# Performance work log

Measured on AMD Instinct MI355X. Metric: run time of the kernel, lower is better.

The kernel has to match this reference:

```python
import jax, jax.numpy as jnp
import numpy as np

COMMITMENT_COST = 0.25


def setup_inputs() -> dict:
    key = jax.random.key(0)
    k1, k2 = jax.random.split(key)
    B, K, D = 1048576, 16, 64
    z = jax.random.normal(k1, (B, D), dtype=jnp.float32)
    # nn.Embedding init: uniform(-1/K, 1/K)
    embedding = jax.random.uniform(k2, (K, D), dtype=jnp.float32,
                                   minval=-1.0 / K, maxval=1.0 / K)
    return {"z": z, "embedding": embedding}


def reference(z, embedding):
    # squared L2 distances: ||z||^2 + ||e||^2 - 2 z e^T  -> [B, K]
    distances = (jnp.sum(z * z, axis=1, keepdims=True)
                 + jnp.sum(embedding * embedding, axis=1)
                 - 2.0 * jnp.matmul(z, embedding.T))
    encoding_indices = jnp.argmin(distances, axis=1)           # [B]
    quantized = embedding[encoding_indices]                    # [B, D]

    commitment_loss = jnp.mean((z - jax.lax.stop_gradient(quantized)) ** 2)
    embedding_loss = jnp.mean((jax.lax.stop_gradient(z) - quantized) ** 2)
    vq_loss = embedding_loss + COMMITMENT_COST * commitment_loss

    # straight-through estimator
    quantized = z + jax.lax.stop_gradient(quantized - z)
    return quantized, encoding_indices, vq_loss
```

## Files before the change

### kernel.cpp

```cpp
#include <hip/hip_runtime.h>

#define B_ROWS 1048576
#define K_CODES 16
#define D_DIM 64

constexpr int BLOCK = 256;
constexpr int GRID  = 2048;

__global__ __launch_bounds__(BLOCK)
void vq_main(const float* __restrict__ z,
             const float* __restrict__ emb,
             float* __restrict__ out_q,
             float* __restrict__ out_idx,
             float* __restrict__ partials)
{
    __shared__ __align__(16) float s_emb[K_CODES * D_DIM];
    __shared__ float s_se[K_CODES];
    __shared__ float s_w[BLOCK / 64];

    const int t = threadIdx.x;

    ((float4*)s_emb)[t] = ((const float4*)emb)[t];
    __syncthreads();

    if (t < K_CODES) {
        float s = 0.f;
        #pragma unroll
        for (int c = 0; c < D_DIM; ++c) {
            float e = s_emb[t * D_DIM + c];
            s = fmaf(e, e, s);
        }
        s_se[t] = s;
    }
    __syncthreads();

    const int j = t & 15;
    float4 ereg[16];
    #pragma unroll
    for (int k = 0; k < 16; ++k)
        ereg[k] = *(const float4*)&s_emb[k * D_DIM + j * 4];
    const float se_j = s_se[j];

    float lossacc = 0.f;

    const int gid    = (blockIdx.x * BLOCK + t) >> 4;
    const int stride = (GRID * BLOCK) >> 4;

    for (int row = gid; row < B_ROWS; row += stride) {
        const float4 zv = *(const float4*)&z[(size_t)row * D_DIM + j * 4];

        float p[16];
        #pragma unroll
        for (int k = 0; k < 16; ++k) {
            float4 e = ereg[k];
            p[k] = fmaf(zv.w, e.w, fmaf(zv.z, e.z, fmaf(zv.y, e.y, zv.x * e.x)));
        }
        float szp = fmaf(zv.w, zv.w, fmaf(zv.z, zv.z, fmaf(zv.y, zv.y, zv.x * zv.x)));
        szp += __shfl_xor(szp, 8, 64);
        szp += __shfl_xor(szp, 4, 64);
        szp += __shfl_xor(szp, 2, 64);
        szp += __shfl_xor(szp, 1, 64);

        bool hi = (j & 8) != 0;
        float r8[8];
        #pragma unroll
        for (int i = 0; i < 8; ++i) {
            float sendv = hi ? p[i] : p[i + 8];
            float keepv = hi ? p[i + 8] : p[i];
            r8[i] = keepv + __shfl_xor(sendv, 8, 64);
        }
        hi = (j & 4) != 0;
        float r4[4];
        #pragma unroll
        for (int i = 0; i < 4; ++i) {
            float sendv = hi ? r8[i] : r8[i + 4];
            float keepv = hi ? r8[i + 4] : r8[i];
            r4[i] = keepv + __shfl_xor(sendv, 4, 64);
        }
        hi = (j & 2) != 0;
        float r2[2];
        #pragma unroll
        for (int i = 0; i < 2; ++i) {
            float sendv = hi ? r2[i] : r4[i + 2];
            (void)sendv;
        }
        {
            float sendv0 = hi ? r4[0] : r4[2];
            float keepv0 = hi ? r4[2] : r4[0];
            r2[0] = keepv0 + __shfl_xor(sendv0, 2, 64);
            float sendv1 = hi ? r4[1] : r4[3];
            float keepv1 = hi ? r4[3] : r4[1];
            r2[1] = keepv1 + __shfl_xor(sendv1, 2, 64);
        }
        hi = (j & 1) != 0;
        float dot;
        {
            float sendv = hi ? r2[0] : r2[1];
            float keepv = hi ? r2[1] : r2[0];
            dot = keepv + __shfl_xor(sendv, 1, 64);
        }

        const float tt = szp + se_j;
        const float d  = tt - 2.0f * dot;

        float vmin = d;
        vmin = fminf(vmin, __shfl_xor(vmin, 1, 64));
        vmin = fminf(vmin, __shfl_xor(vmin, 2, 64));
        vmin = fminf(vmin, __shfl_xor(vmin, 4, 64));
        vmin = fminf(vmin, __shfl_xor(vmin, 8, 64));
        unsigned long long bal = __ballot(d == vmin);
        unsigned int mask = (unsigned int)((bal >> (t & 48)) & 0xFFFFull);
        int kmin = __ffs(mask) - 1;

        const float4 qv = *(const float4*)&s_emb[kmin * D_DIM + j * 4];

        float dx = zv.x - qv.x; lossacc = fmaf(dx, dx, lossacc);
        dx = zv.y - qv.y;       lossacc = fmaf(dx, dx, lossacc);
        dx = zv.z - qv.z;       lossacc = fmaf(dx, dx, lossacc);
        dx = zv.w - qv.w;       lossacc = fmaf(dx, dx, lossacc);

        *(float4*)&out_q[(size_t)row * D_DIM + j * 4] = qv;
        if (j == 0) out_idx[row] = (float)kmin;
    }

    lossacc += __shfl_xor(lossacc, 32, 64);
    lossacc += __shfl_xor(lossacc, 16, 64);
    lossacc += __shfl_xor(lossacc, 8, 64);
    lossacc += __shfl_xor(lossacc, 4, 64);
    lossacc += __shfl_xor(lossacc, 2, 64);
    lossacc += __shfl_xor(lossacc, 1, 64);
    if ((t & 63) == 0) s_w[t >> 6] = lossacc;
    __syncthreads();
    if (t == 0) partials[blockIdx.x] = (s_w[0] + s_w[1]) + (s_w[2] + s_w[3]);
}

__global__ void vq_finalize(const float* __restrict__ partials, int n,
                            float* __restrict__ out_loss)
{
    __shared__ float sw[4];
    float s = 0.f;
    for (int i = threadIdx.x; i < n; i += 256) s += partials[i];
    s += __shfl_xor(s, 32, 64);
    s += __shfl_xor(s, 16, 64);
    s += __shfl_xor(s, 8, 64);
    s += __shfl_xor(s, 4, 64);
    s += __shfl_xor(s, 2, 64);
    s += __shfl_xor(s, 1, 64);
    if ((threadIdx.x & 63) == 0) sw[threadIdx.x >> 6] = s;
    __syncthreads();
    if (threadIdx.x == 0) {
        float tot = (sw[0] + sw[1]) + (sw[2] + sw[3]);
        *out_loss = tot * (1.25f / (float)(B_ROWS * (size_t)D_DIM));
    }
}

extern "C" void kernel_launch(void* const* d_in, const int* in_sizes, int n_in,
                              void* d_out, int out_size, void* d_ws, size_t ws_size,
                              hipStream_t stream)
{
    const float* z   = (const float*)d_in[0];
    const float* emb = (const float*)d_in[1];
    float* out      = (float*)d_out;
    float* out_q    = out;
    float* out_idx  = out + (size_t)B_ROWS * D_DIM;
    float* out_loss = out_idx + B_ROWS;
    float* partials = (float*)d_ws;

    vq_main<<<GRID, BLOCK, 0, stream>>>(z, emb, out_q, out_idx, partials);
    vq_finalize<<<1, 256, 0, stream>>>(partials, GRID, out_loss);
}
```

Before: 122.8 us.

## Use DPP/swizzle butterfly reduction with XOR-permuted codebook and prefetch next row

Cross-lane shuffles (ds_bpermute) are replaced with DPP quad-permutes for xor 1/2 and ds_swizzle for xor 4/8. The codebook registers are stored XOR-permuted by lane, so the transpose-reduction becomes a plain butterfly without select operations. The next row's z vector is software-prefetched into registers so its load overlaps the current row's compute. The kernel is memory-bound, so the lighter instruction work and the latency hiding may only help modestly. The extra prefetch registers add pressure on an already large register set.

Result: faster. 114.2 us (-7.1%).

```diff
diff --git a/kernel.cpp b/kernel.cpp
--- a/kernel.cpp
+++ b/kernel.cpp
@@ -6,6 +6,25 @@
 
 constexpr int BLOCK = 256;
 constexpr int GRID  = 2048;
+
+__device__ __forceinline__ float xor1_dpp(float x) {
+    return __builtin_bit_cast(float,
+        __builtin_amdgcn_update_dpp(0, __builtin_bit_cast(int, x), 0xB1 ,
+                                    0xF, 0xF, true));
+}
+__device__ __forceinline__ float xor2_dpp(float x) {
+    return __builtin_bit_cast(float,
+        __builtin_amdgcn_update_dpp(0, __builtin_bit_cast(int, x), 0x4E ,
+                                    0xF, 0xF, true));
+}
+__device__ __forceinline__ float xor4_sw(float x) {
+    return __builtin_bit_cast(float,
+        __builtin_amdgcn_ds_swizzle(__builtin_bit_cast(int, x), 0x101F));
+}
+__device__ __forceinline__ float xor8_sw(float x) {
+    return __builtin_bit_cast(float,
+        __builtin_amdgcn_ds_swizzle(__builtin_bit_cast(int, x), 0x201F));
+}
 
 __global__ __launch_bounds__(BLOCK)
 void vq_main(const float* __restrict__ z,
@@ -37,8 +56,8 @@
     const int j = t & 15;
     float4 ereg[16];
     #pragma unroll
-    for (int k = 0; k < 16; ++k)
-        ereg[k] = *(const float4*)&s_emb[k * D_DIM + j * 4];
+    for (int r = 0; r < 16; ++r)
+        ereg[r] = *(const float4*)&s_emb[((r ^ j) * D_DIM) + j * 4];
     const float se_j = s_se[j];
 
     float lossacc = 0.f;
@@ -46,68 +65,44 @@
     const int gid    = (blockIdx.x * BLOCK + t) >> 4;
     const int stride = (GRID * BLOCK) >> 4;
 
-    for (int row = gid; row < B_ROWS; row += stride) {
-        const float4 zv = *(const float4*)&z[(size_t)row * D_DIM + j * 4];
+    int row = gid;
+    float4 zv = *(const float4*)&z[(size_t)row * D_DIM + j * 4];
+
+    while (row < B_ROWS) {
+        const int nrow = row + stride;
+        float4 zn = zv;
+        if (nrow < B_ROWS)
+            zn = *(const float4*)&z[(size_t)nrow * D_DIM + j * 4];
 
         float p[16];
         #pragma unroll
-        for (int k = 0; k < 16; ++k) {
-            float4 e = ereg[k];
-            p[k] = fmaf(zv.w, e.w, fmaf(zv.z, e.z, fmaf(zv.y, e.y, zv.x * e.x)));
-        }
-        float szp = fmaf(zv.w, zv.w, fmaf(zv.z, zv.z, fmaf(zv.y, zv.y, zv.x * zv.x)));
-        szp += __shfl_xor(szp, 8, 64);
-        szp += __shfl_xor(szp, 4, 64);
-        szp += __shfl_xor(szp, 2, 64);
-        szp += __shfl_xor(szp, 1, 64);
-
-        bool hi = (j & 8) != 0;
-        float r8[8];
-        #pragma unroll
-        for (int i = 0; i < 8; ++i) {
-            float sendv = hi ? p[i] : p[i + 8];
-            float keepv = hi ? p[i + 8] : p[i];
-            r8[i] = keepv + __shfl_xor(sendv, 8, 64);
-        }
-        hi = (j & 4) != 0;
-        float r4[4];
-        #pragma unroll
-        for (int i = 0; i < 4; ++i) {
-            float sendv = hi ? r8[i] : r8[i + 4];
-            float keepv = hi ? r8[i + 4] : r8[i];
-            r4[i] = keepv + __shfl_xor(sendv, 4, 64);
-        }
-        hi = (j & 2) != 0;
-        float r2[2];
-        #pragma unroll
-        for (int i = 0; i < 2; ++i) {
-            float sendv = hi ? r2[i] : r4[i + 2];
-            (void)sendv;
-        }
-        {
-            float sendv0 = hi ? r4[0] : r4[2];
-            float keepv0 = hi ? r4[2] : r4[0];
-            r2[0] = keepv0 + __shfl_xor(sendv0, 2, 64);
-            float sendv1 = hi ? r4[1] : r4[3];
-            float keepv1 = hi ? r4[3] : r4[1];
-            r2[1] = keepv1 + __shfl_xor(sendv1, 2, 64);
-        }
-        hi = (j & 1) != 0;
-        float dot;
-        {
-            float sendv = hi ? r2[0] : r2[1];
-            float keepv = hi ? r2[1] : r2[0];
-            dot = keepv + __shfl_xor(sendv, 1, 64);
+        for (int r = 0; r < 16; ++r) {
+            float4 e = ereg[r];
+            p[r] = fmaf(zv.w, e.w, fmaf(zv.z, e.z, fmaf(zv.y, e.y, zv.x * e.x)));
         }
 
-        const float tt = szp + se_j;
-        const float d  = tt - 2.0f * dot;
+        float szp = fmaf(zv.w, zv.w, fmaf(zv.z, zv.z, fmaf(zv.y, zv.y, zv.x * zv.x)));
+        szp += xor1_dpp(szp);
+        szp += xor2_dpp(szp);
+        szp += xor4_sw(szp);
+        szp += xor8_sw(szp);
+
+        #pragma unroll
+        for (int r = 0; r < 16; r += 2)  p[r] += xor1_dpp(p[r + 1]);
+        #pragma unroll
+        for (int r = 0; r < 16; r += 4)  p[r] += xor2_dpp(p[r + 2]);
+        #pragma unroll
+        for (int r = 0; r < 16; r += 8)  p[r] += xor4_sw(p[r + 4]);
+        p[0] += xor8_sw(p[8]);
+        const float dot = p[0];
+
+        const float d = (szp + se_j) - 2.0f * dot;
 
         float vmin = d;
-        vmin = fminf(vmin, __shfl_xor(vmin, 1, 64));
-        vmin = fminf(vmin, __shfl_xor(vmin, 2, 64));
-        vmin = fminf(vmin, __shfl_xor(vmin, 4, 64));
-        vmin = fminf(vmin, __shfl_xor(vmin, 8, 64));
+        vmin = fminf(vmin, xor1_dpp(vmin));
+        vmin = fminf(vmin, xor2_dpp(vmin));
+        vmin = fminf(vmin, xor4_sw(vmin));
+        vmin = fminf(vmin, xor8_sw(vmin));
         unsigned long long bal = __ballot(d == vmin);
         unsigned int mask = (unsigned int)((bal >> (t & 48)) & 0xFFFFull);
         int kmin = __ffs(mask) - 1;
@@ -121,6 +116,9 @@
 
         *(float4*)&out_q[(size_t)row * D_DIM + j * 4] = qv;
         if (j == 0) out_idx[row] = (float)kmin;
+
+        zv  = zn;
+        row = nrow;
     }
 
     lossacc += __shfl_xor(lossacc, 32, 64);
```
